# Kernel tuning notes

Measured on AMD Instinct MI355X. Metric: run time of the kernel, lower is better.

The kernel has to match this reference:

```python
import jax, jax.numpy as jnp
import numpy as np

NEG_SLOPE = 0.2

def _gatv2(x_src, x_dst, src, dst, Wl, bl, Wr, br, att, bias, num_dst, edge_feat=None, We=None):
    # PyG GATv2Conv (heads=1, add_self_loops=False, eval mode -> no dropout)
    xl = x_src @ Wl + bl                      # [Ns, C] lin_l on source
    xr = x_dst @ Wr + br                      # [Nd, C] lin_r on target
    m = xl[src] + xr[dst]                     # [E, C]
    if edge_feat is not None:
        m = m + edge_feat @ We                # lin_edge (bias=False)
    e = jax.nn.leaky_relu(m, NEG_SLOPE) @ att # [E] attention logits
    emax = jax.ops.segment_max(e, dst, num_segments=num_dst)
    ee = jnp.exp(e - emax[dst])
    denom = jax.ops.segment_sum(ee, dst, num_segments=num_dst)
    alpha = ee / jnp.maximum(denom[dst], 1e-16)
    out = jax.ops.segment_sum(alpha[:, None] * xl[src], dst, num_segments=num_dst)
    return out + bias


def setup_inputs() -> dict:
    key = jax.random.key(0)
    N_OP, N_M, N_A = 50000, 5000, 2000
    C_OP, C_M, C_A = 256, 128, 128
    E_OO, E_OM, E_MA, E_DIM = 200000, 200000, 60000, 8
    ks = jax.random.split(key, 40)
    i = iter(range(40))
    def nrm(shape, fan_in):
        return jax.random.normal(ks[next(i)], shape, dtype=jnp.float32) / np.sqrt(fan_in)
    inp = {}
    inp['x_op'] = jax.random.normal(ks[next(i)], (N_OP, C_OP), dtype=jnp.float32)
    inp['x_m'] = jax.random.normal(ks[next(i)], (N_M, C_M), dtype=jnp.float32)
    inp['x_a'] = jax.random.normal(ks[next(i)], (N_A, C_A), dtype=jnp.float32)
    inp['ei_pred'] = jax.random.randint(ks[next(i)], (2, E_OO), 0, N_OP)
    inp['ei_succ'] = jax.random.randint(ks[next(i)], (2, E_OO), 0, N_OP)
    inp['src_o2m'] = jax.random.randint(ks[next(i)], (E_OM,), 0, N_OP)
    inp['dst_o2m'] = jax.random.randint(ks[next(i)], (E_OM,), 0, N_M)
    inp['src_m2a'] = jax.random.randint(ks[next(i)], (E_MA,), 0, N_M)
    inp['dst_m2a'] = jax.random.randint(ks[next(i)], (E_MA,), 0, N_A)
    inp['ea_m2a'] = jax.random.normal(ks[next(i)], (E_MA, E_DIM), dtype=jnp.float32)
    for name, c_in_src, c_in_dst, c_out in [('pred', C_OP, C_OP, C_OP), ('succ', C_OP, C_OP, C_OP), ('o2m', C_OP, C_M, C_M), ('m2a', C_M, C_A, C_A)]:
        inp[f'Wl_{name}'] = nrm((c_in_src, c_out), c_in_src)
        inp[f'bl_{name}'] = jnp.zeros((c_out,), jnp.float32)
        inp[f'Wr_{name}'] = nrm((c_in_dst, c_out), c_in_dst)
        inp[f'br_{name}'] = jnp.zeros((c_out,), jnp.float32)
        inp[f'att_{name}'] = nrm((c_out,), c_out)
        inp[f'b_{name}'] = jnp.zeros((c_out,), jnp.float32)
    inp['We_m2a'] = nrm((E_DIM, C_A), E_DIM)
    return inp


def reference(x_op, x_m, x_a, ei_pred, ei_succ, src_o2m, dst_o2m, src_m2a, dst_m2a, ea_m2a,
              Wl_pred, bl_pred, Wr_pred, br_pred, att_pred, b_pred,
              Wl_succ, bl_succ, Wr_succ, br_succ, att_succ, b_succ,
              Wl_o2m, bl_o2m, Wr_o2m, br_o2m, att_o2m, b_o2m,
              Wl_m2a, bl_m2a, Wr_m2a, br_m2a, att_m2a, b_m2a, We_m2a):
    N_OP, N_M, N_A = x_op.shape[0], x_m.shape[0], x_a.shape[0]
    # operation_relation_extract: two op->op GATv2 convs, HeteroConv sum-aggregated
    f_pred = _gatv2(x_op, x_op, ei_pred[0], ei_pred[1], Wl_pred, bl_pred, Wr_pred, br_pred, att_pred, b_pred, N_OP)
    f_succ = _gatv2(x_op, x_op, ei_succ[0], ei_succ[1], Wl_succ, bl_succ, Wr_succ, br_succ, att_succ, b_succ, N_OP)
    # hetero_relation_extract
    f_mach = _gatv2(x_op, x_m, src_o2m, dst_o2m, Wl_o2m, bl_o2m, Wr_o2m, br_o2m, att_o2m, b_o2m, N_M)
    f_agv = _gatv2(x_m, x_a, src_m2a, dst_m2a, Wl_m2a, bl_m2a, Wr_m2a, br_m2a, att_m2a, b_m2a, N_A, edge_feat=ea_m2a, We=We_m2a)
    # residual sum across relation outputs per node type
    out_op = x_op + f_pred + f_succ
    out_m = x_m + f_mach
    out_a = x_a + f_agv
    return (out_op, out_m, out_a)
```

## Files before the change

kernel.cpp:

```cpp
#include <hip/hip_runtime.h>

#define N_OP   50000
#define N_M    5000
#define N_A    2000
#define C_OP   256
#define C_M    128
#define C_A    128
#define E_OO   200000
#define E_OM   200000
#define E_MA   60000
#define E_DIM  8

#define OUT_OP_OFF 0
#define OUT_M_OFF  (N_OP * C_OP)
#define OUT_A_OFF  (N_OP * C_OP + N_M * C_M)

typedef short bf16x8 __attribute__((ext_vector_type(8)));
typedef float f32x4 __attribute__((ext_vector_type(4)));
typedef __attribute__((address_space(1))) const unsigned gu32;
typedef __attribute__((address_space(3))) unsigned lu32;

__device__ __forceinline__ unsigned short f2bf(float f) {
    unsigned u = __float_as_uint(f);
    unsigned r = (u + 0x7FFFu + ((u >> 16) & 1u)) >> 16;
    return (unsigned short)r;
}
__device__ __forceinline__ float bf2f(unsigned short h) {
    return __uint_as_float(((unsigned)h) << 16);
}

#define NTOT 107000
#define ETOT 660000

#define I3_OP (N_OP * C_OP / 4)
#define I3_M  (I3_OP + N_M * C_M / 4)
#define I3_A  (I3_M + N_A * C_A / 4)

#define PK_P   131072
#define PK_S   262144
#define PK_OL  294912
#define PK_OR  311296
#define PK_ML  327680
#define PK_MR  344064
#define PK_BP  344576
#define PK_BS  345088

#define PREP_HIST_BLK 645
#define PREP_INIT_BLK (I3_A / 256)
#define PREP_PACK_BLK (PK_BS / 256)
#define PREP_FRONT    (6 * PREP_HIST_BLK)
#define PREP_TOTAL    (PREP_HIST_BLK + PREP_INIT_BLK + PREP_PACK_BLK)

__device__ __forceinline__ void init_one(const float* __restrict__ x,
                                         const float* __restrict__ b1,
                                         float* __restrict__ out,
                                         unsigned short* __restrict__ xc,
                                         int i, int cmask) {
    float4 v = ((const float4*)x)[i];
    const int cb = i & cmask;
    float4 b = ((const float4*)b1)[cb];
    float4 o;
    o.x = v.x + b.x; o.y = v.y + b.y; o.z = v.z + b.z; o.w = v.w + b.w;
    ((float4*)out)[i] = o;
    ushort4 r;
    r.x = f2bf(v.x); r.y = f2bf(v.y); r.z = f2bf(v.z); r.w = f2bf(v.w);
    ((ushort4*)xc)[i] = r;
}

__device__ __forceinline__ void hist_one(
    int i,
    const int* __restrict__ dP, const int* __restrict__ dS,
    const int* __restrict__ dO, const int* __restrict__ dA,
    int* __restrict__ cP, int* __restrict__ cS,
    int* __restrict__ cO, int* __restrict__ cA, int* __restrict__ rk) {
    if (i < 200000)      rk[i] = atomicAdd(&cP[dP[i]], 1);
    else if (i < 400000) rk[i] = atomicAdd(&cS[dS[i - 200000]], 1);
    else if (i < 600000) rk[i] = atomicAdd(&cO[dO[i - 400000]], 1);
    else if (i < ETOT)   rk[i] = atomicAdd(&cA[dA[i - 600000]], 1);
}

__global__ void prep_all(
    const int* __restrict__ dP, const int* __restrict__ dS,
    const int* __restrict__ dO, const int* __restrict__ dA,
    int* __restrict__ cP, int* __restrict__ cS,
    int* __restrict__ cO, int* __restrict__ cA, int* __restrict__ rk,
    const float* __restrict__ x_op, const float* __restrict__ x_m,
    const float* __restrict__ x_a,
    const float* __restrict__ bO, const float* __restrict__ bA,
    float* __restrict__ out_m, float* __restrict__ out_a,
    unsigned short* __restrict__ xcop, unsigned short* __restrict__ xcm,
    unsigned short* __restrict__ xca,
    const float* __restrict__ WlP, const float* __restrict__ WrP,
    const float* __restrict__ WlS, const float* __restrict__ WrS,
    const float* __restrict__ WOl, const float* __restrict__ WOr,
    const float* __restrict__ WMl, const float* __restrict__ WMr,
    const float* __restrict__ blP, const float* __restrict__ brP,
    const float* __restrict__ blS, const float* __restrict__ brS,
    unsigned short* __restrict__ BtP, unsigned short* __restrict__ BtS,
    unsigned short* __restrict__ BtOL, unsigned short* __restrict__ BtOR,
    unsigned short* __restrict__ BtML, unsigned short* __restrict__ BtMR,
    float* __restrict__ biasP, float* __restrict__ biasS) {
    const int b = blockIdx.x;
    const int tid = threadIdx.x;
    int ib;
    if (b < PREP_FRONT) {
        if ((b % 6) == 5) {
            const int h = b / 6;
            const int base = h * 1024 + tid;
            hist_one(base,       dP, dS, dO, dA, cP, cS, cO, cA, rk);
            hist_one(base + 256, dP, dS, dO, dA, cP, cS, cO, cA, rk);
            hist_one(base + 512, dP, dS, dO, dA, cP, cS, cO, cA, rk);
            hist_one(base + 768, dP, dS, dO, dA, cP, cS, cO, cA, rk);
            return;
        }
        ib = b - b / 6;
    } else {
        ib = b - PREP_HIST_BLK;
    }
    if (ib < PREP_INIT_BLK) {
        int i = ib * 256 + tid;
        if (i < I3_OP) {
            float4 v = ((const float4*)x_op)[i];
            ushort4 r;
            r.x = f2bf(v.x); r.y = f2bf(v.y); r.z = f2bf(v.z); r.w = f2bf(v.w);
            ((ushort4*)xcop)[i] = r;
        } else if (i < I3_M) {
            init_one(x_m, bO, out_m, xcm, i - I3_OP, 31);
        } else {
            init_one(x_a, bA, out_a, xca, i - I3_M, 31);
        }
    } else {
        int i = (ib - PREP_INIT_BLK) * 256 + tid;
        if (i < PK_P) {
            int n = i >> 8, k = i & 255;
            BtP[i] = f2bf((n < 256) ? WlP[k * 256 + n] : WrP[k * 256 + (n - 256)]);
        } else if (i < PK_S) {
            int j = i - PK_P; int n = j >> 8, k = j & 255;
            BtS[j] = f2bf((n < 256) ? WlS[k * 256 + n] : WrS[k * 256 + (n - 256)]);
        } else if (i < PK_OL) {
            int j = i - PK_S; int n = j >> 8, k = j & 255;
            BtOL[j] = f2bf(WOl[k * 128 + n]);
        } else if (i < PK_OR) {
            int j = i - PK_OL; int n = j >> 7, k = j & 127;
            BtOR[j] = f2bf(WOr[k * 128 + n]);
        } else if (i < PK_ML) {
            int j = i - PK_OR; int n = j >> 7, k = j & 127;
            BtML[j] = f2bf(WMl[k * 128 + n]);
        } else if (i < PK_MR) {
            int j = i - PK_ML; int n = j >> 7, k = j & 127;
            BtMR[j] = f2bf(WMr[k * 128 + n]);
        } else if (i < PK_BP) {
            int j = i - PK_MR;
            biasP[j] = (j < 256) ? blP[j] : brP[j - 256];
        } else if (i < PK_BS) {
            int j = i - PK_BP;
            biasS[j] = (j < 256) ? blS[j] : brS[j - 256];
        }
    }
}

__device__ __forceinline__ void gload_lds16(const void* g, void* l) {
    __builtin_amdgcn_global_load_lds((gu32*)g, (lu32*)l, 16, 0, 0);
}

__device__ __forceinline__ void gemm_body(
    const unsigned short* __restrict__ A, const unsigned short* __restrict__ Bt,
    const float* __restrict__ bias, unsigned short* __restrict__ C,
    int M, int K, int ldc, int bx, int by,
    unsigned short (&As)[128 * 64], unsigned short (&Bs)[128 * 64]) {
    const int tid  = threadIdx.x;
    const int lane = tid & 63;
    const int wid  = tid >> 6;
    const int m0   = bx * 128;
    const int n0   = by * 128;

    f32x4 acc[4][4] = {};

    const int srow   = tid >> 3;
    const int scolb  = (tid & 7) * 16;
    const int scole  = (scolb ^ ((srow & 7) << 4)) >> 1;

    int grA[4], grB[4];
#pragma unroll
    for (int i = 0; i < 4; ++i) {
        int gr = m0 + i * 32 + srow;
        grA[i] = (gr < M) ? gr : M - 1;
        grB[i] = n0 + i * 32 + srow;
    }

    const int nt = K >> 6;
    const int wr = (wid >> 1) * 64;
    const int wc = (wid & 1) * 64;

    for (int t = 0; t < nt; ++t) {
#pragma unroll
        for (int i = 0; i < 4; ++i)
            gload_lds16(A + (size_t)grA[i] * K + t * 64 + scole, &As[i * 2048 + tid * 8]);
#pragma unroll
        for (int i = 0; i < 4; ++i)
            gload_lds16(Bt + (size_t)grB[i] * K + t * 64 + scole, &Bs[i * 2048 + tid * 8]);
        asm volatile("s_waitcnt vmcnt(0)" ::: "memory");
        __syncthreads();
#pragma unroll
        for (int kh = 0; kh < 2; ++kh) {
            const int kob = kh * 64 + (lane >> 4) * 16;
            bf16x8 a[4], b[4];
#pragma unroll
            for (int mi = 0; mi < 4; ++mi) {
                const int row = wr + mi * 16 + (lane & 15);
                a[mi] = *(const bf16x8*)((const char*)As + row * 128 +
                                         (kob ^ ((row & 7) << 4)));
            }
#pragma unroll
            for (int ni = 0; ni < 4; ++ni) {
                const int row = wc + ni * 16 + (lane & 15);
                b[ni] = *(const bf16x8*)((const char*)Bs + row * 128 +
                                         (kob ^ ((row & 7) << 4)));
            }
#pragma unroll
            for (int mi = 0; mi < 4; ++mi)
#pragma unroll
                for (int ni = 0; ni < 4; ++ni)
                    acc[mi][ni] = __builtin_amdgcn_mfma_f32_16x16x32_bf16(
                        a[mi], b[ni], acc[mi][ni], 0, 0, 0);
        }
        __syncthreads();
    }

    const int crow = (lane >> 4) * 4;
    const int ccol = lane & 15;
    float bcol[4];
#pragma unroll
    for (int ni = 0; ni < 4; ++ni) bcol[ni] = bias[n0 + wc + ni * 16 + ccol];
#pragma unroll
    for (int mi = 0; mi < 4; ++mi) {
#pragma unroll
        for (int j = 0; j < 4; ++j) {
            const int row = m0 + wr + mi * 16 + crow + j;
            if (row < M) {
                unsigned short* pc = C + (size_t)row * ldc + n0 + wc + ccol;
#pragma unroll
                for (int ni = 0; ni < 4; ++ni)
                    pc[ni * 16] = f2bf(acc[mi][ni][j] + bcol[ni]);
            }
        }
    }
}

__global__ __launch_bounds__(256) void mfma_gemm(
    const unsigned short* __restrict__ A, const unsigned short* __restrict__ Bt,
    const float* __restrict__ bias, unsigned short* __restrict__ C,
    int M, int K, int ldc) {
    __shared__ unsigned short As[128 * 64];
    __shared__ unsigned short Bs[128 * 64];
    const int b = blockIdx.x;
    const int xcd = b & 7, pos = b >> 3;
    const int lb = ((xcd < 4) ? xcd * 196 : 4 * 196 + (xcd - 4) * 195) + pos;
    gemm_body(A, Bt, bias, C, M, K, ldc, lb >> 2, lb & 3, As, Bs);
}

#define MT_OPB 391
#define MT_MB  40
#define MT_AB  16
#define GM_SWZ   1955
#define GM_SMALL 2051
#define GM_TOTAL 4630

__global__ __launch_bounds__(256) void gemm_multi(
    const unsigned short* __restrict__ xc_op, const unsigned short* __restrict__ xc_m,
    const unsigned short* __restrict__ xc_a,
    const unsigned short* __restrict__ BtP, const float* __restrict__ biasP,
    unsigned short* __restrict__ H,
    const unsigned short* __restrict__ BtOL, const unsigned short* __restrict__ BtOR,
    const unsigned short* __restrict__ BtML, const unsigned short* __restrict__ BtMR,
    const float* __restrict__ blO, const float* __restrict__ brO,
    const float* __restrict__ blM, const float* __restrict__ brM,
    unsigned short* __restrict__ xlbO, unsigned short* __restrict__ xrbO,
    unsigned short* __restrict__ xlbM, unsigned short* __restrict__ xrbM,
    const int* __restrict__ sP, const int* __restrict__ dP,
    const int* __restrict__ sS, const int* __restrict__ dS,
    const int* __restrict__ sO, const int* __restrict__ dO,
    const int* __restrict__ sA, const int* __restrict__ dA,
    const int* __restrict__ pP, const int* __restrict__ pS,
    const int* __restrict__ pO, const int* __restrict__ pA,
    const int* __restrict__ rk,
    int* __restrict__ srP, int* __restrict__ srS,
    int* __restrict__ srO, int* __restrict__ srA, int* __restrict__ eiA) {
    __shared__ unsigned short As[128 * 64];
    __shared__ unsigned short Bs[128 * 64];
    const int b = blockIdx.x;
    if (b < GM_SWZ) {
        const int xcd = b & 7, pos = b >> 3;
        const int lb = ((xcd < 3) ? xcd * 245 : 3 * 245 + (xcd - 3) * 244) + pos;
        const int bx = lb / 5, role = lb - bx * 5;
        if (role < 4)
            gemm_body(xc_op, BtP, biasP, H, N_OP, 256, 512, bx, role, As, Bs);
        else
            gemm_body(xc_op, BtOL, blO, xlbO, N_OP, 256, 128, bx, 0, As, Bs);
    } else if (b < GM_SMALL) {
        const int idx = b - GM_SWZ;
        if (idx < MT_MB)
            gemm_body(xc_m, BtOR, brO, xrbO, N_M, 128, 128, idx, 0, As, Bs);
        else if (idx < 2 * MT_MB)
            gemm_body(xc_m, BtML, blM, xlbM, N_M, 128, 128, idx - MT_MB, 0, As, Bs);
        else
            gemm_body(xc_a, BtMR, brM, xrbM, N_A, 128, 128, idx - 2 * MT_MB, 0, As, Bs);
    } else {
        const int i = (b - GM_SMALL) * 256 + (int)threadIdx.x;
        if (i < 200000) {
            srP[pP[dP[i]] + rk[i]] = sP[i];
        } else if (i < 400000) {
            const int j = i - 200000;
            srS[pS[dS[j]] + rk[i]] = sS[j];
        } else if (i < 600000) {
            const int j = i - 400000;
            srO[pO[dO[j]] + rk[i]] = sO[j];
        } else if (i < ETOT) {
            const int j = i - 600000;
            const int pos = pA[dA[j]] + rk[i];
            srA[pos] = sA[j];
            eiA[pos] = j;
        }
    }
}

#define NB_P 49
#define NB_S 49
#define NB_O 5
#define NB_A 2

__global__ void scan_blk4(const int* __restrict__ cP, const int* __restrict__ cS,
                          const int* __restrict__ cO, const int* __restrict__ cA,
                          int* __restrict__ pP, int* __restrict__ pS,
                          int* __restrict__ pO, int* __restrict__ pA,
                          int* __restrict__ bsum) {
    __shared__ int smem[1024];
    int b = blockIdx.x;
    const int* cnt; int* ptr; int n; int bo;
    if (b < NB_P)                { cnt = cP; ptr = pP; n = 50000; bo = 0; }
    else if (b < NB_P + NB_S)    { cnt = cS; ptr = pS; n = 50000; bo = 64;  b -= NB_P; }
    else if (b < NB_P + NB_S + NB_O) { cnt = cO; ptr = pO; n = 5000; bo = 128; b -= NB_P + NB_S; }
    else                         { cnt = cA; ptr = pA; n = 2000; bo = 192; b -= NB_P + NB_S + NB_O; }
    const int tid = threadIdx.x;
    const int i = b * 1024 + tid;
    const int v = (i < n) ? cnt[i] : 0;
    smem[tid] = v;
    __syncthreads();
    for (int o = 1; o < 1024; o <<= 1) {
        int t = (tid >= o) ? smem[tid - o] : 0;
        __syncthreads();
        smem[tid] += t;
        __syncthreads();
    }
    if (i < n) ptr[i] = smem[tid] - v;
    if (tid == 1023) bsum[bo + b] = smem[1023];
}

__global__ void scan_tops4(const int* __restrict__ bsum, int* __restrict__ boff,
                           int* __restrict__ pP, int* __restrict__ pS,
                           int* __restrict__ pO, int* __restrict__ pA) {
    __shared__ int smem[1024];
    const int seg = blockIdx.x;
    const int nb = (seg < 2) ? 49 : (seg == 2 ? 5 : 2);
    const int off = seg * 64;
    int* ptr_n = (seg == 0) ? pP + 50000 : (seg == 1) ? pS + 50000
               : (seg == 2) ? pO + 5000 : pA + 2000;
    const int tid = threadIdx.x;
    const int v = (tid < nb) ? bsum[off + tid] : 0;
    smem[tid] = v;
    __syncthreads();
    for (int o = 1; o < 1024; o <<= 1) {
        int t = (tid >= o) ? smem[tid - o] : 0;
        __syncthreads();
        smem[tid] += t;
        __syncthreads();
    }
    if (tid < nb) boff[off + tid] = smem[tid] - v;
    if (tid == 1023) *ptr_n = smem[1023];
}

__global__ void scan_add4(int* __restrict__ pP, int* __restrict__ pS,
                          int* __restrict__ pO, int* __restrict__ pA,
                          const int* __restrict__ boff) {
    int i = blockIdx.x * blockDim.x + threadIdx.x;
    int* ptr; int loc; int off;
    if (i < 50000)       { ptr = pP; loc = i;          off = 0; }
    else if (i < 100000) { ptr = pS; loc = i - 50000;  off = 64; }
    else if (i < 105000) { ptr = pO; loc = i - 100000; off = 128; }
    else if (i < NTOT)   { ptr = pA; loc = i - 105000; off = 192; }
    else return;
    ptr[loc] += boff[off + (loc >> 10)];
}

template <bool INIT>
__device__ __forceinline__ void csr_body2(
    const unsigned short* __restrict__ xl, int ldl,
    const unsigned short* __restrict__ xr, int ldr,
    const float* __restrict__ att,
    const int* __restrict__ ptr, const int* __restrict__ srcs,
    const float* __restrict__ xbase, const float* __restrict__ b1,
    const float* __restrict__ b2,
    float* __restrict__ out, int n) {
    const int tid = threadIdx.x;
    const int node = blockIdx.x * 8 + (tid >> 5);
    if (node >= n) return;
    const int gl = tid & 31;
    const int beg = ptr[node], end = ptr[node + 1];
    if (!INIT && beg == end) return;

    constexpr int V = 8;
    const int c0 = gl * V;

    float runM = -3.0e38f, runS = 0.0f;
    float acc[V] = {};

    if (INIT || beg < end) {
        float av[V], rvf[V];
        {
            const unsigned short* pr = xr + (size_t)node * ldr + c0;
            unsigned short rv[V];
            *(uint4*)rv = *(const uint4*)pr;
#pragma unroll
            for (int v4 = 0; v4 < V / 4; ++v4)
                *(float4*)(av + v4 * 4) = ((const float4*)(att + c0))[v4];
#pragma unroll
            for (int v = 0; v < V; ++v) rvf[v] = bf2f(rv[v]);
        }

        if (beg < end) {
            unsigned short lv[V];
            {
                const unsigned short* pl = xl + (size_t)srcs[beg] * ldl + c0;
                *(uint4*)lv = *(const uint4*)pl;
            }
            for (int j = beg; j < end; ++j) {
                float cf[V];
#pragma unroll
                for (int v = 0; v < V; ++v) cf[v] = bf2f(lv[v]);
                if (j + 1 < end) {
                    const unsigned short* pl = xl + (size_t)srcs[j + 1] * ldl + c0;
                    *(uint4*)lv = *(const uint4*)pl;
                }

                float part = 0.0f;
#pragma unroll
                for (int v = 0; v < V; ++v) {
                    float m = cf[v] + rvf[v];
                    m = (m >= 0.0f) ? m : 0.2f * m;
                    part += m * av[v];
                }
                part += __shfl_xor(part, 1, 64);
                part += __shfl_xor(part, 2, 64);
                part += __shfl_xor(part, 4, 64);
                part += __shfl_xor(part, 8, 64);
                part += __shfl_xor(part, 16, 64);

                const float newM = fmaxf(runM, part);
                const float sc = __expf(runM - newM);
                const float e1 = __expf(part - newM);
                runS = runS * sc + e1;
                runM = newM;
#pragma unroll
                for (int v = 0; v < V; ++v) acc[v] = acc[v] * sc + e1 * cf[v];
            }
        }
    }

    const float inv = 1.0f / fmaxf(runS, 1e-16f);
    float* po = out + (size_t)node * 256 + c0;
    if (INIT) {
        const float* px = xbase + (size_t)node * 256 + c0;
#pragma unroll
        for (int v4 = 0; v4 < V / 4; ++v4) {
            float4 xv = ((const float4*)px)[v4];
            float4 bv1 = ((const float4*)(b1 + c0))[v4];
            float4 bv2 = ((const float4*)(b2 + c0))[v4];
            float4 o;
            o.x = xv.x + bv1.x + bv2.x + acc[v4 * 4 + 0] * inv;
            o.y = xv.y + bv1.y + bv2.y + acc[v4 * 4 + 1] * inv;
            o.z = xv.z + bv1.z + bv2.z + acc[v4 * 4 + 2] * inv;
            o.w = xv.w + bv1.w + bv2.w + acc[v4 * 4 + 3] * inv;
            ((float4*)po)[v4] = o;
        }
    } else {
#pragma unroll
        for (int v4 = 0; v4 < V / 4; ++v4) {
            float4 o = ((float4*)po)[v4];
            o.x += acc[v4 * 4 + 0] * inv;
            o.y += acc[v4 * 4 + 1] * inv;
            o.z += acc[v4 * 4 + 2] * inv;
            o.w += acc[v4 * 4 + 3] * inv;
            ((float4*)po)[v4] = o;
        }
    }
}

__global__ void csr_init2(const unsigned short* __restrict__ xl, int ldl,
                          const unsigned short* __restrict__ xr, int ldr,
                          const float* __restrict__ att,
                          const int* __restrict__ ptr, const int* __restrict__ srcs,
                          const float* __restrict__ xbase,
                          const float* __restrict__ b1, const float* __restrict__ b2,
                          float* __restrict__ out, int n) {
    csr_body2<true>(xl, ldl, xr, ldr, att, ptr, srcs, xbase, b1, b2, out, n);
}

__global__ void csr_serial2(const unsigned short* __restrict__ xl, int ldl,
                            const unsigned short* __restrict__ xr, int ldr,
                            const float* __restrict__ att,
                            const int* __restrict__ ptr, const int* __restrict__ srcs,
                            float* __restrict__ out, int n) {
    csr_body2<false>(xl, ldl, xr, ldr, att, ptr, srcs, nullptr, nullptr, nullptr, out, n);
}

template <bool EF>
__device__ __forceinline__ void csrg_body(
    const unsigned short* __restrict__ xl, const unsigned short* __restrict__ xr,
    const float* __restrict__ att,
    const int* __restrict__ ptr, const int* __restrict__ srcs,
    const int* __restrict__ eid, const float* __restrict__ ea,
    const float* __restrict__ We,
    float* __restrict__ out, int n, int blk) {
    const int node = blk * 4 + ((int)threadIdx.x >> 6);
    if (node >= n) return;
    const int lane = threadIdx.x & 63;
    const int grp  = lane >> 4;
    const int sl   = lane & 15;
    const int beg = ptr[node], end = ptr[node + 1];
    if (beg == end) return;

    constexpr int W = 8;
    const int c0 = sl * W;

    float av[W], rvf[W];
    {
        const unsigned short* pr = xr + (size_t)node * 128 + c0;
        unsigned short rv[W];
        *(uint4*)rv = *(const uint4*)pr;
#pragma unroll
        for (int v4 = 0; v4 < 2; ++v4)
            *(float4*)(av + v4 * 4) = ((const float4*)(att + c0))[v4];
#pragma unroll
        for (int v = 0; v < W; ++v) rvf[v] = bf2f(rv[v]);
    }

    float wreg[64];
    if constexpr (EF) {
#pragma unroll
        for (int k = 0; k < 8; ++k) {
            *(float4*)(wreg + k * 8)     = *(const float4*)(We + k * 128 + c0);
            *(float4*)(wreg + k * 8 + 4) = *(const float4*)(We + k * 128 + c0 + 4);
        }
    }

    float runM = -3.0e38f, runS = 0.0f;
    float acc[W] = {};

    for (int cb = beg; cb < end; cb += 4) {
        const int j = cb + grp;
        const bool act = (j < end);
        const int js = act ? j : end - 1;
        const int s = srcs[js];

        const unsigned short* pl = xl + (size_t)s * 128 + c0;
        unsigned short lv[W];
        *(uint4*)lv = *(const uint4*)pl;
        float cf[W];
#pragma unroll
        for (int v = 0; v < W; ++v) cf[v] = bf2f(lv[v]);

        float part = 0.0f;
        if constexpr (EF) {
            const int oe = eid[js];
            float eav[8];
            *(float4*)eav       = *(const float4*)(ea + (size_t)oe * 8);
            *(float4*)(eav + 4) = *(const float4*)(ea + (size_t)oe * 8 + 4);
#pragma unroll
            for (int v = 0; v < W; ++v) {
                float efv = eav[0] * wreg[v];
#pragma unroll
                for (int k = 1; k < 8; ++k) efv += eav[k] * wreg[k * 8 + v];
                float m = cf[v] + rvf[v] + efv;
                m = (m >= 0.0f) ? m : 0.2f * m;
                part += m * av[v];
            }
        } else {
#pragma unroll
            for (int v = 0; v < W; ++v) {
                float m = cf[v] + rvf[v];
                m = (m >= 0.0f) ? m : 0.2f * m;
                part += m * av[v];
            }
        }
        part += __shfl_xor(part, 1, 64);
        part += __shfl_xor(part, 2, 64);
        part += __shfl_xor(part, 4, 64);
        part += __shfl_xor(part, 8, 64);
        if (!act) part = -3.0e38f;

        float cm = fmaxf(part, __shfl_xor(part, 16, 64));
        cm = fmaxf(cm, __shfl_xor(cm, 32, 64));

        if (cm > runM) {
            const float sc = __expf(runM - cm);
            runS *= sc;
#pragma unroll
            for (int v = 0; v < W; ++v) acc[v] *= sc;
            runM = cm;
        }
        const float w = act ? __expf(part - runM) : 0.0f;
        float cs = w + __shfl_xor(w, 16, 64);
        cs += __shfl_xor(cs, 32, 64);
        runS += cs;
#pragma unroll
        for (int v = 0; v < W; ++v) acc[v] += w * cf[v];
    }

#pragma unroll
    for (int v = 0; v < W; ++v) acc[v] += __shfl_xor(acc[v], 16, 64);
#pragma unroll
    for (int v = 0; v < W; ++v) acc[v] += __shfl_xor(acc[v], 32, 64);

    const float inv = 1.0f / fmaxf(runS, 1e-16f);
    if (grp == 0) {
        float* po = out + (size_t)node * 128 + c0;
#pragma unroll
        for (int v4 = 0; v4 < 2; ++v4) {
            float4 o = ((float4*)po)[v4];
            o.x += acc[v4 * 4 + 0] * inv;
            o.y += acc[v4 * 4 + 1] * inv;
            o.z += acc[v4 * 4 + 2] * inv;
            o.w += acc[v4 * 4 + 3] * inv;
            ((float4*)po)[v4] = o;
        }
    }
}

#define CP_O 1250
__global__ void csr_pair(
    const unsigned short* __restrict__ xlbO, const unsigned short* __restrict__ xrbO,
    const float* __restrict__ attO,
    const int* __restrict__ ptrO, const int* __restrict__ srcO,
    float* __restrict__ out_m,
    const unsigned short* __restrict__ xlbM, const unsigned short* __restrict__ xrbM,
    const float* __restrict__ attA,
    const int* __restrict__ ptrA, const int* __restrict__ srcA,
    const int* __restrict__ eidA, const float* __restrict__ ea,
    const float* __restrict__ We, float* __restrict__ out_a) {
    const int b = blockIdx.x;
    if (b < CP_O)
        csrg_body<false>(xlbO, xrbO, attO, ptrO, srcO, nullptr, nullptr, nullptr,
                         out_m, N_M, b);
    else
        csrg_body<true>(xlbM, xrbM, attA, ptrA, srcA, eidA, ea, We,
                        out_a, N_A, b - CP_O);
}

#define F_H      0
#define F_XCOP   12800000
#define F_XCM    19200000
#define F_XCA    19520000
#define F_BTP    19648000
#define F_BTS    19713536
#define F_BTOL   19779072
#define F_BTOR   19795456
#define F_BTML   19803648
#define F_BTMR   19811840
#define F_BIASP  19820032
#define F_BIASS  19820544
#define F_CNT4   19821056
#define F_BSUM   19928056
#define F_BOFF   19928312
#define F_PTR_P  19928568
#define F_SRC_P  19978569
#define F_PTR_S  20178569
#define F_SRC_S  20228570
#define F_PTR_O  20428570
#define F_SRC_O  20433571
#define F_PTR_A  20633571
#define F_SRC_A  20635572
#define F_EID_A  20695572
#define F_RANK   20755572
#define F_XLO    21415572
#define F_XRO    24615572
#define F_XLM    24935572
#define F_XRM    25255572

extern "C" void kernel_launch(void* const* d_in, const int* in_sizes, int n_in,
                              void* d_out, int out_size, void* d_ws, size_t ws_size,
                              hipStream_t stream) {
    const float* x_op    = (const float*)d_in[0];
    const float* x_m     = (const float*)d_in[1];
    const float* x_a     = (const float*)d_in[2];
    const int*   ei_pred = (const int*)d_in[3];
    const int*   ei_succ = (const int*)d_in[4];
    const int*   src_o2m = (const int*)d_in[5];
    const int*   dst_o2m = (const int*)d_in[6];
    const int*   src_m2a = (const int*)d_in[7];
    const int*   dst_m2a = (const int*)d_in[8];
    const float* ea_m2a  = (const float*)d_in[9];

    const float* Wl_pred = (const float*)d_in[10];
    const float* bl_pred = (const float*)d_in[11];
    const float* Wr_pred = (const float*)d_in[12];
    const float* br_pred = (const float*)d_in[13];
    const float* att_pred= (const float*)d_in[14];
    const float* b_pred  = (const float*)d_in[15];

    const float* Wl_succ = (const float*)d_in[16];
    const float* bl_succ = (const float*)d_in[17];
    const float* Wr_succ = (const float*)d_in[18];
    const float* br_succ = (const float*)d_in[19];
    const float* att_succ= (const float*)d_in[20];
    const float* b_succ  = (const float*)d_in[21];

    const float* Wl_o2m  = (const float*)d_in[22];
    const float* bl_o2m  = (const float*)d_in[23];
    const float* Wr_o2m  = (const float*)d_in[24];
    const float* br_o2m  = (const float*)d_in[25];
    const float* att_o2m = (const float*)d_in[26];
    const float* b_o2m   = (const float*)d_in[27];

    const float* Wl_m2a  = (const float*)d_in[28];
    const float* bl_m2a  = (const float*)d_in[29];
    const float* Wr_m2a  = (const float*)d_in[30];
    const float* br_m2a  = (const float*)d_in[31];
    const float* att_m2a = (const float*)d_in[32];
    const float* b_m2a   = (const float*)d_in[33];
    const float* We_m2a  = (const float*)d_in[34];

    float* ws = (float*)d_ws;
    unsigned short* H     = (unsigned short*)(ws + F_H);
    unsigned short* xc_op = (unsigned short*)(ws + F_XCOP);
    unsigned short* xc_m  = (unsigned short*)(ws + F_XCM);
    unsigned short* xc_a  = (unsigned short*)(ws + F_XCA);
    unsigned short* BtP   = (unsigned short*)(ws + F_BTP);
    unsigned short* BtS   = (unsigned short*)(ws + F_BTS);
    unsigned short* BtOL  = (unsigned short*)(ws + F_BTOL);
    unsigned short* BtOR  = (unsigned short*)(ws + F_BTOR);
    unsigned short* BtML  = (unsigned short*)(ws + F_BTML);
    unsigned short* BtMR  = (unsigned short*)(ws + F_BTMR);
    float* biasP = ws + F_BIASP;
    float* biasS = ws + F_BIASS;
    int* cntP = (int*)(ws + F_CNT4);
    int* cntS = cntP + 50000;
    int* cntO = cntP + 100000;
    int* cntA = cntP + 105000;
    int* bsum = (int*)(ws + F_BSUM);
    int* boff = (int*)(ws + F_BOFF);
    int* ptrP = (int*)(ws + F_PTR_P); int* srcP = (int*)(ws + F_SRC_P);
    int* ptrS = (int*)(ws + F_PTR_S); int* srcS = (int*)(ws + F_SRC_S);
    int* ptrO = (int*)(ws + F_PTR_O); int* srcO = (int*)(ws + F_SRC_O);
    int* ptrA = (int*)(ws + F_PTR_A); int* srcA = (int*)(ws + F_SRC_A);
    int* eidA = (int*)(ws + F_EID_A);
    int* rk   = (int*)(ws + F_RANK);
    unsigned short* xlbO = (unsigned short*)(ws + F_XLO);
    unsigned short* xrbO = (unsigned short*)(ws + F_XRO);
    unsigned short* xlbM = (unsigned short*)(ws + F_XLM);
    unsigned short* xrbM = (unsigned short*)(ws + F_XRM);

    float* out_op = (float*)d_out + OUT_OP_OFF;
    float* out_m  = (float*)d_out + OUT_M_OFF;
    float* out_a  = (float*)d_out + OUT_A_OFF;

    hipMemsetAsync(cntP, 0, NTOT * sizeof(int), stream);

    prep_all<<<PREP_TOTAL, 256, 0, stream>>>(
        ei_pred + E_OO, ei_succ + E_OO, dst_o2m, dst_m2a,
        cntP, cntS, cntO, cntA, rk,
        x_op, x_m, x_a, b_o2m, b_m2a,
        out_m, out_a, xc_op, xc_m, xc_a,
        Wl_pred, Wr_pred, Wl_succ, Wr_succ, Wl_o2m, Wr_o2m, Wl_m2a, Wr_m2a,
        bl_pred, br_pred, bl_succ, br_succ,
        BtP, BtS, BtOL, BtOR, BtML, BtMR, biasP, biasS);

    scan_blk4<<<NB_P + NB_S + NB_O + NB_A, 1024, 0, stream>>>(cntP, cntS, cntO, cntA,
                                                              ptrP, ptrS, ptrO, ptrA, bsum);
    scan_tops4<<<4, 1024, 0, stream>>>(bsum, boff, ptrP, ptrS, ptrO, ptrA);
    scan_add4<<<(NTOT + 255) / 256, 256, 0, stream>>>(ptrP, ptrS, ptrO, ptrA, boff);

    gemm_multi<<<GM_TOTAL, 256, 0, stream>>>(
        xc_op, xc_m, xc_a, BtP, biasP, H,
        BtOL, BtOR, BtML, BtMR, bl_o2m, br_o2m, bl_m2a, br_m2a,
        xlbO, xrbO, xlbM, xrbM,
        ei_pred, ei_pred + E_OO, ei_succ, ei_succ + E_OO,
        src_o2m, dst_o2m, src_m2a, dst_m2a,
        ptrP, ptrS, ptrO, ptrA, rk,
        srcP, srcS, srcO, srcA, eidA);

    csr_init2<<<(N_OP + 7) / 8, 256, 0, stream>>>(H, 512, H + 256, 512,
                                                  att_pred, ptrP, srcP,
                                                  x_op, b_pred, b_succ,
                                                  out_op, N_OP);

    mfma_gemm<<<MT_OPB * 4, 256, 0, stream>>>(xc_op, BtS, biasS, H, N_OP, 256, 512);

    csr_serial2<<<(N_OP + 7) / 8, 256, 0, stream>>>(H, 512, H + 256, 512,
                                                    att_succ, ptrS, srcS, out_op, N_OP);

    csr_pair<<<CP_O + (N_A + 3) / 4, 256, 0, stream>>>(
        xlbO, xrbO, att_o2m, ptrO, srcO, out_m,
        xlbM, xrbM, att_m2a, ptrA, srcA, eidA, ea_m2a, We_m2a, out_a);
}
```

Baseline: 251.6 us.

## Prefetch next edge gather in CSR attention loop and split pair kernel

Software-pipelines the per-edge loop in the CSR GATv2 aggregation body: the source feature row and edge attributes for the next batch of four edges are loaded while the current batch is processed, to hide gather latency. The fused csr_pair launch is also split into two separate kernels, one for o2m and one for m2a. Splitting adds a launch and removes the overlap of the two relations within a single grid, while the prefetch raises register pressure.

```diff
diff --git a/kernel.cpp b/kernel.cpp
--- a/kernel.cpp
+++ b/kernel.cpp
@@ -556,30 +556,50 @@
     float runM = -3.0e38f, runS = 0.0f;
     float acc[W] = {};
 
+    unsigned short lv[W];
+    float eav[8];
+    {
+        const int j0 = beg + grp;
+        const int js0 = (j0 < end) ? j0 : end - 1;
+        *(uint4*)lv = *(const uint4*)(xl + (size_t)srcs[js0] * 128 + c0);
+        if constexpr (EF) {
+            const int oe = eid[js0];
+            *(float4*)eav       = *(const float4*)(ea + (size_t)oe * 8);
+            *(float4*)(eav + 4) = *(const float4*)(ea + (size_t)oe * 8 + 4);
+        }
+    }
+
     for (int cb = beg; cb < end; cb += 4) {
         const int j = cb + grp;
         const bool act = (j < end);
-        const int js = act ? j : end - 1;
-        const int s = srcs[js];
-
-        const unsigned short* pl = xl + (size_t)s * 128 + c0;
-        unsigned short lv[W];
-        *(uint4*)lv = *(const uint4*)pl;
+
         float cf[W];
 #pragma unroll
         for (int v = 0; v < W; ++v) cf[v] = bf2f(lv[v]);
+        float eavc[8];
+        if constexpr (EF) {
+#pragma unroll
+            for (int k = 0; k < 8; ++k) eavc[k] = eav[k];
+        }
+
+        if (cb + 4 < end) {
+            const int jn = cb + 4 + grp;
+            const int jsn = (jn < end) ? jn : end - 1;
+            *(uint4*)lv = *(const uint4*)(xl + (size_t)srcs[jsn] * 128 + c0);
+            if constexpr (EF) {
+                const int oe = eid[jsn];
+                *(float4*)eav       = *(const float4*)(ea + (size_t)oe * 8);
+                *(float4*)(eav + 4) = *(const float4*)(ea + (size_t)oe * 8 + 4);
+            }
+        }
 
         float part = 0.0f;
         if constexpr (EF) {
-            const int oe = eid[js];
-            float eav[8];
-            *(float4*)eav       = *(const float4*)(ea + (size_t)oe * 8);
-            *(float4*)(eav + 4) = *(const float4*)(ea + (size_t)oe * 8 + 4);
 #pragma unroll
             for (int v = 0; v < W; ++v) {
-                float efv = eav[0] * wreg[v];
-#pragma unroll
-                for (int k = 1; k < 8; ++k) efv += eav[k] * wreg[k * 8 + v];
+                float efv = eavc[0] * wreg[v];
+#pragma unroll
+                for (int k = 1; k < 8; ++k) efv += eavc[k] * wreg[k * 8 + v];
                 float m = cf[v] + rvf[v] + efv;
                 m = (m >= 0.0f) ? m : 0.2f * m;
                 part += m * av[v];
@@ -636,24 +656,23 @@
     }
 }
 
-#define CP_O 1250
-__global__ void csr_pair(
-    const unsigned short* __restrict__ xlbO, const unsigned short* __restrict__ xrbO,
-    const float* __restrict__ attO,
-    const int* __restrict__ ptrO, const int* __restrict__ srcO,
-    float* __restrict__ out_m,
-    const unsigned short* __restrict__ xlbM, const unsigned short* __restrict__ xrbM,
-    const float* __restrict__ attA,
-    const int* __restrict__ ptrA, const int* __restrict__ srcA,
-    const int* __restrict__ eidA, const float* __restrict__ ea,
+__global__ void csr_o2m(
+    const unsigned short* __restrict__ xlb, const unsigned short* __restrict__ xrb,
+    const float* __restrict__ att,
+    const int* __restrict__ ptr, const int* __restrict__ srcs,
+    float* __restrict__ out_m) {
+    csrg_body<false>(xlb, xrb, att, ptr, srcs, nullptr, nullptr, nullptr,
+                     out_m, N_M, blockIdx.x);
+}
+
+__global__ void csr_m2a(
+    const unsigned short* __restrict__ xlb, const unsigned short* __restrict__ xrb,
+    const float* __restrict__ att,
+    const int* __restrict__ ptr, const int* __restrict__ srcs,
+    const int* __restrict__ eid, const float* __restrict__ ea,
     const float* __restrict__ We, float* __restrict__ out_a) {
-    const int b = blockIdx.x;
-    if (b < CP_O)
-        csrg_body<false>(xlbO, xrbO, attO, ptrO, srcO, nullptr, nullptr, nullptr,
-                         out_m, N_M, b);
-    else
-        csrg_body<true>(xlbM, xrbM, attA, ptrA, srcA, eidA, ea, We,
-                        out_a, N_A, b - CP_O);
+    csrg_body<true>(xlb, xrb, att, ptr, srcs, eid, ea, We,
+                    out_a, N_A, blockIdx.x);
 }
 
 #define F_H      0
@@ -798,7 +817,9 @@
     csr_serial2<<<(N_OP + 7) / 8, 256, 0, stream>>>(H, 512, H + 256, 512,
                                                     att_succ, ptrS, srcS, out_op, N_OP);
 
-    csr_pair<<<CP_O + (N_A + 3) / 4, 256, 0, stream>>>(
-        xlbO, xrbO, att_o2m, ptrO, srcO, out_m,
-        xlbM, xrbM, att_m2a, ptrA, srcA, eidA, ea_m2a, We_m2a, out_a);
-}
+    csr_o2m<<<(N_M + 3) / 4, 256, 0, stream>>>(xlbO, xrbO, att_o2m,
+                                               ptrO, srcO, out_m);
+
+    csr_m2a<<<(N_A + 3) / 4, 256, 0, stream>>>(xlbM, xrbM, att_m2a,
+                                               ptrA, srcA, eidA, ea_m2a, We_m2a, out_a);
+}
```

New measurement: 257.2 us. 2.2% more time.
